# Optimization experiments

Hardware: AMD Instinct MI355X
Metric: run time of the kernel (lower is better)

The kernel has to match this reference:

```python
import jax, jax.numpy as jnp
import numpy as np

H = 12          # num attention heads
DH = 64         # head size (768 / 12)
THRESHOLD = 0.05


def setup_inputs() -> dict:
    key = jax.random.key(0)
    ks = jax.random.split(key, 13)
    B, S, D = 128, 197, 768
    s = 0.02
    return {
        "hidden_states": jax.random.normal(ks[0], (B, S, D), jnp.float32),
        "Wq": jax.random.normal(ks[1], (D, D), jnp.float32) * s,
        "bq": jax.random.normal(ks[2], (D,), jnp.float32) * s,
        "Wk": jax.random.normal(ks[3], (D, D), jnp.float32) * s,
        "bk": jax.random.normal(ks[4], (D,), jnp.float32) * s,
        "Wv": jax.random.normal(ks[5], (D, D), jnp.float32) * s,
        "bv": jax.random.normal(ks[6], (D,), jnp.float32) * s,
        "Wd": jax.random.normal(ks[7], (D, D), jnp.float32) * s,
        "bd": jax.random.normal(ks[8], (D,), jnp.float32) * s,
        "W1": jax.random.normal(ks[9], (D, 64), jnp.float32) * s,
        "b1": jax.random.normal(ks[10], (64,), jnp.float32) * s,
        "W2": jax.random.normal(ks[11], (64, 1), jnp.float32) * s,
        "b2": jax.random.normal(ks[12], (1,), jnp.float32) * s,
    }


def reference(hidden_states, Wq, bq, Wk, bk, Wv, bv, Wd, bd, W1, b1, W2, b2):
    B, S, D = hidden_states.shape
    # --- DHS scoring MLP on patch tokens (exclude CLS), keep_cls=True path ---
    h = jax.nn.relu(hidden_states[:, 1:] @ W1 + b1)        # [B, S-1, 64]
    mlp_out = jax.nn.sigmoid(h @ W2 + b2)[..., 0]          # [B, S-1]
    patch_mask = mlp_out >= THRESHOLD                      # [B, S-1]
    cls_col = jnp.ones((B, 1), dtype=bool)
    mask = jnp.concatenate([cls_col, patch_mask], axis=1)  # [B, S]

    # --- full self-attention; pruning queries only removes rows, keys/values
    # are never pruned, so computing all rows and masking is equivalent ---
    q = (hidden_states @ Wq + bq).reshape(B, S, H, DH)
    k = (hidden_states @ Wk + bk).reshape(B, S, H, DH)
    v = (hidden_states @ Wv + bv).reshape(B, S, H, DH)
    scores = jnp.einsum("bqhd,bkhd->bhqk", q, k) / jnp.sqrt(jnp.float32(DH))
    probs = jax.nn.softmax(scores, axis=-1)                # dropout p=0.0 (eval)
    ctx = jnp.einsum("bhqk,bkhd->bqhd", probs, v).reshape(B, S, D)
    attn_out = (ctx @ Wd + bd) + ctx                       # dense + residual-to-self_outputs

    # scatter-assign: output[i][mask[i]] = attn_out rows for kept tokens
    output = jnp.where(mask[..., None], attn_out, hidden_states)
    return output
```

## Files before the change

### kernel.cpp

```cpp
#include <hip/hip_runtime.h>
#include <hip/hip_bf16.h>

#define HN 12
#define DHD 64
#define BB 128
#define SQ 197
#define DD 768
#define TOK (BB*SQ)
#define SP 224
#define SPS 232

using short8  = __attribute__((ext_vector_type(8))) short;
using floatx4 = __attribute__((ext_vector_type(4))) float;

__device__ __forceinline__ float bf2f(short v) {
    union { unsigned int u; float f; } x;
    x.u = ((unsigned int)(unsigned short)v) << 16;
    return x.f;
}
__device__ __forceinline__ short f2bf(float f) {
    union { float f; unsigned int u; } x; x.f = f;
    unsigned int u = x.u;
    u += 0x7fffu + ((u >> 16) & 1u);
    return (short)(u >> 16);
}
__device__ __forceinline__ float ldf(const void* p, size_t i, bool isf32) {
    return isf32 ? ((const float*)p)[i] : bf2f(((const short*)p)[i]);
}
__device__ __forceinline__ void gload_lds16(const short* g, short* l) {
    __builtin_amdgcn_global_load_lds(
        (const __attribute__((address_space(1))) void*)g,
        (__attribute__((address_space(3))) void*)l, 16, 0, 0);
}

__global__ __launch_bounds__(256) void detect_kernel(
        const short* __restrict__ wq, float* __restrict__ flag) {
    __shared__ int cnt;
    if (threadIdx.x == 0) cnt = 0;
    __syncthreads();
    int local = 0;
    for (int j = 0; j < 16; j++) {
        int i = threadIdx.x * 16 + j;
        unsigned int u = (unsigned short)wq[2 * i];
        unsigned int e = (u >> 7) & 0xFF;
        if (e < 64 || e >= 192) local++;
    }
    for (int d = 1; d < 64; d <<= 1) local += __shfl_xor(local, d, 64);
    if ((threadIdx.x & 63) == 0) atomicAdd(&cnt, local);
    __syncthreads();
    if (threadIdx.x == 0) *flag = (cnt > 256) ? 1.f : 0.f;
}

__global__ void sentinel_kernel(short* out, int n, float code) {
    int i = blockIdx.x * 256 + threadIdx.x;
    if (i < n) out[i] = (i == 0) ? f2bf(code) : (short)0;
}

__global__ __launch_bounds__(256) void prep_kernel(
        const void* __restrict__ Wq, const void* __restrict__ Wk,
        const void* __restrict__ Wv, const void* __restrict__ Wd,
        const void* __restrict__ bq, const void* __restrict__ bk,
        const void* __restrict__ bv, const void* __restrict__ bd,
        const void* __restrict__ W1, const void* __restrict__ b1,
        const void* __restrict__ W2, const void* __restrict__ b2,
        short* __restrict__ WqkvT, short* __restrict__ WdT,
        short* __restrict__ W1T, float* __restrict__ bcat,
        const float* __restrict__ flag) {
    __shared__ short tile[64][72];
    bool isf32 = (*flag != 0.f);
    int blk = blockIdx.x;
    int tid = threadIdx.x;
    int r = tid >> 2, c0 = (tid & 3) << 4;
    const void* W;
    size_t stride;
    int ti, tj, w = 0;
    if (blk < 576) {
        w = blk / 144;
        int t = blk % 144;
        ti = t / 12; tj = t % 12;
        W = (w == 0) ? Wq : (w == 1) ? Wk : (w == 2) ? Wv : Wd;
        stride = DD;
    } else {
        ti = blk - 576; tj = 0;
        W = W1;
        stride = 64;
    }
    for (int c = 0; c < 16; c++)
        tile[r][c0 + c] =
            f2bf(ldf(W, (size_t)(ti * 64 + r) * stride + tj * 64 + c0 + c, isf32));
    __syncthreads();
    short* out;
    if (blk < 576)
        out = (w < 3)
            ? WqkvT + ((size_t)(w * DD + tj * 64 + r)) * DD + ti * 64
            : WdT   + ((size_t)(tj * 64 + r)) * DD + ti * 64;
    else
        out = W1T + (size_t)r * DD + ti * 64;
    for (int h = 0; h < 2; h++) {
        short8 v;
        #pragma unroll
        for (int c = 0; c < 8; c++) v[c] = tile[c0 + h * 8 + c][r];
        *(short8*)&out[c0 + h * 8] = v;
    }
    if (blk == 0) {
        for (int i = tid; i < DD; i += 256) {
            bcat[i]          = ldf(bq, i, isf32);
            bcat[DD + i]     = ldf(bk, i, isf32);
            bcat[2 * DD + i] = ldf(bv, i, isf32);
            bcat[3 * DD + i] = ldf(bd, i, isf32);
        }
        if (tid < 64) {
            bcat[4 * DD + tid]      = ldf(b1, tid, isf32);
            bcat[4 * DD + 64 + tid] = ldf(W2, tid, isf32);
        }
        if (tid == 0) bcat[4 * DD + 128] = ldf(b2, 0, isf32);
    }
}

__global__ __launch_bounds__(256) void mask_gemm(
        const void* __restrict__ hs, const short* __restrict__ W1T,
        const float* __restrict__ bvec, float* __restrict__ mask,
        short* __restrict__ hsb, const float* __restrict__ flag) {
    __shared__ __align__(16) short As[64 * 32];
    __shared__ __align__(16) short Bs[64 * 32];
    bool isf32 = (*flag != 0.f);
    int tid = threadIdx.x, lane = tid & 63, wave = tid >> 6;
    int quad = lane >> 4, l16 = lane & 15;
    int tok0 = blockIdx.x * 64;

    int arow = tid >> 2, achk = tid & 3;
    int acol = ((achk ^ ((arow >> 1) & 3)) << 3);
    const short* Bg = W1T + (size_t)arow * DD +
                      (((achk ^ ((arow >> 1) & 3)) << 3));
    short* Bl = Bs + wave * 512;
    int fcol = ((quad ^ ((l16 >> 1) & 3)) << 3);

    floatx4 acc[4] = {};
    for (int k0 = 0; k0 < DD; k0 += 32) {
        gload_lds16(Bg + k0, Bl);
        size_t gidx = (size_t)(tok0 + arow) * DD + k0 + achk * 8;
        short8 s;
        if (isf32) {
            const float* hf = (const float*)hs;
            float4 f0 = *(const float4*)&hf[gidx];
            float4 f1 = *(const float4*)&hf[gidx + 4];
            s[0]=f2bf(f0.x); s[1]=f2bf(f0.y); s[2]=f2bf(f0.z); s[3]=f2bf(f0.w);
            s[4]=f2bf(f1.x); s[5]=f2bf(f1.y); s[6]=f2bf(f1.z); s[7]=f2bf(f1.w);
        } else {
            s = *(const short8*)&((const short*)hs)[gidx];
        }
        *(short8*)&hsb[gidx] = s;
        *(short8*)&As[(arow << 5) + acol] = s;
        __syncthreads();
        short8 af = *(const short8*)&As[((wave * 16 + l16) << 5) + fcol];
        #pragma unroll
        for (int j = 0; j < 4; j++) {
            short8 bf8 = *(const short8*)&Bs[((j * 16 + l16) << 5) + fcol];
            acc[j] = __builtin_amdgcn_mfma_f32_16x16x32_bf16(af, bf8, acc[j], 0, 0, 0);
        }
        __syncthreads();
    }

    const float* b1f = bvec + 4 * DD;
    const float* w2f = bvec + 4 * DD + 64;
    float b2v = bvec[4 * DD + 128];
    float partial[4] = {0.f, 0.f, 0.f, 0.f};
    #pragma unroll
    for (int j = 0; j < 4; j++) {
        int n = j * 16 + l16;
        float b1v = b1f[n], w2v = w2f[n];
        #pragma unroll
        for (int r = 0; r < 4; r++) {
            float hv = fmaxf(acc[j][r] + b1v, 0.f);
            partial[r] += hv * w2v;
        }
    }
    for (int d = 1; d < 16; d <<= 1)
        #pragma unroll
        for (int r = 0; r < 4; r++)
            partial[r] += __shfl_xor(partial[r], d, 64);
    if (l16 == 0) {
        #pragma unroll
        for (int r = 0; r < 4; r++) {
            int tokr = tok0 + wave * 16 + quad * 4 + r;
            float m = 1.f;
            if (tokr % SQ != 0) {
                float sg = 1.f / (1.f + __expf(-(partial[r] + b2v)));
                m = (sg >= 0.05f) ? 1.f : 0.f;
            }
            mask[tokr] = m;
        }
    }
}

template <int MODE>
__global__ __launch_bounds__(512, 4) void gemm128(
        const short* __restrict__ A, const short* __restrict__ BT,
        const float* __restrict__ bias, void* __restrict__ C,
        int m0g, int Mreal, int N,
        const float* __restrict__ mask, const short* __restrict__ resid,
        const void* __restrict__ hs, const float* __restrict__ flag) {
    constexpr int K = DD;
    constexpr int BK = 64;
    __shared__ __align__(16) short As[128 * BK];
    __shared__ __align__(16) short Bs[128 * BK];
    int tiles_n = N >> 7;
    int nwg = gridDim.x, bid = blockIdx.x;
    int qq = nwg >> 3, rr = nwg & 7, xcd = bid & 7, lid = bid >> 3;
    int wg = (xcd < rr ? xcd * (qq + 1) : rr * (qq + 1) + (xcd - rr) * qq) + lid;
    int bm = wg / tiles_n, bn = wg % tiles_n;
    int m0 = bm << 7, n0 = bn << 7;

    int tid = threadIdx.x, lane = tid & 63, wave = tid >> 6;
    int wx = wave & 3, wy = wave >> 2;
    int quad = lane >> 4, l16 = lane & 15, l7 = l16 & 7;

    int slot0 = (wave << 7) + lane;
    int slot1 = slot0 + 64;
    int r0 = slot0 >> 3, c0s = ((slot0 & 7) ^ (r0 & 7)) << 3;
    int r1 = slot1 >> 3, c1s = ((slot1 & 7) ^ (r1 & 7)) << 3;
    int am0 = m0 + r0; if (am0 >= Mreal) am0 = Mreal - 1;
    int am1 = m0 + r1; if (am1 >= Mreal) am1 = Mreal - 1;
    const short* Ag0 = A + (size_t)am0 * K + c0s;
    const short* Ag1 = A + (size_t)am1 * K + c1s;
    const short* Bg0 = BT + (size_t)(n0 + r0) * K + c0s;
    const short* Bg1 = BT + (size_t)(n0 + r1) * K + c1s;
    short* Al0 = As + wave * 1024;
    short* Al1 = Al0 + 512;
    short* Bl0 = Bs + wave * 1024;
    short* Bl1 = Bl0 + 512;

    floatx4 acc[4][2] = {};
    for (int k0 = 0; k0 < K; k0 += BK) {
        gload_lds16(Ag0 + k0, Al0);
        gload_lds16(Ag1 + k0, Al1);
        gload_lds16(Bg0 + k0, Bl0);
        gload_lds16(Bg1 + k0, Bl1);
        __syncthreads();
        #pragma unroll
        for (int ks = 0; ks < 2; ks++) {
            int colo = ((((ks << 2) + quad) ^ l7) << 3);
            short8 af[4], bfr[2];
            #pragma unroll
            for (int i = 0; i < 4; i++)
                af[i] = *(const short8*)&As[(((wy << 6) + (i << 4) + l16) << 6) + colo];
            #pragma unroll
            for (int j = 0; j < 2; j++)
                bfr[j] = *(const short8*)&Bs[(((wx << 5) + (j << 4) + l16) << 6) + colo];
            #pragma unroll
            for (int i = 0; i < 4; i++)
                #pragma unroll
                for (int j = 0; j < 2; j++)
                    acc[i][j] = __builtin_amdgcn_mfma_f32_16x16x32_bf16(
                        af[i], bfr[j], acc[i][j], 0, 0, 0);
        }
        __syncthreads();
    }

    bool isf32 = (MODE == 1) ? (*flag != 0.f) : false;
    #pragma unroll
    for (int i = 0; i < 4; i++)
        #pragma unroll
        for (int j = 0; j < 2; j++) {
            int n = n0 + (wx << 5) + (j << 4) + l16;
            float bb = bias[n];
            #pragma unroll
            for (int r = 0; r < 4; r++) {
                int m = m0 + (wy << 6) + (i << 4) + (quad << 2) + r;
                if (m >= Mreal) continue;
                float v = acc[i][j][r] + bb;
                if (MODE == 0) {
                    ((short*)C)[(size_t)m * N + n] = f2bf(v);
                } else {
                    size_t gm = (size_t)(m0g + m);
                    v += bf2f(resid[(size_t)m * N + n]);
                    if (mask[gm] == 0.f) v = ldf(hs, gm * N + n, isf32);
                    if (isf32) ((float*)C)[gm * N + n] = v;
                    else       ((short*)C)[gm * N + n] = f2bf(v);
                }
            }
        }
}

__global__ __launch_bounds__(256) void attn_kernel(
        const short* __restrict__ qkv, short* __restrict__ ctx) {
    __shared__ __align__(16) short Vt[DHD * SPS];
    __shared__ __align__(16) short P[4 * 16 * SPS];
    int nwg = gridDim.x, bid = blockIdx.x;
    int qq = nwg >> 3, rr = nwg & 7, xcd = bid & 7, lid = bid >> 3;
    int blk = (xcd < rr ? xcd * (qq + 1) : rr * (qq + 1) + (xcd - rr) * qq) + lid;
    int qc = blk & 3;
    int h  = (blk >> 2) % HN;
    int b  = blk / (4 * HN);
    int tid = threadIdx.x, lane = tid & 63, wave = tid >> 6;
    int quad = lane >> 4, l16 = lane & 15;
    const short* base = qkv + (size_t)b * SQ * 2304;

    for (int i = tid; i < SQ * DHD; i += 256) {
        int s = i >> 6, d = i & 63;
        Vt[d * SPS + s] = base[(size_t)s * 2304 + 1536 + h * 64 + d];
    }
    for (int i = tid; i < (SP - SQ) * DHD; i += 256) {
        int s = SQ + i % (SP - SQ), d = i / (SP - SQ);
        Vt[d * SPS + s] = 0;
    }
    __syncthreads();

    int mrow = qc * 64 + wave * 16 + l16;
    if (mrow > SQ - 1) mrow = SQ - 1;
    const short* Qrow = base + (size_t)mrow * 2304 + h * 64;
    short8 aq0 = *(const short8*)(Qrow + quad * 8);
    short8 aq1 = *(const short8*)(Qrow + 32 + quad * 8);

    floatx4 sc[14];
    for (int t = 0; t < 14; t++) {
        int nrow = t * 16 + l16;
        if (nrow > SQ - 1) nrow = SQ - 1;
        const short* Krow = base + (size_t)nrow * 2304 + DD + h * 64;
        short8 b0 = *(const short8*)(Krow + quad * 8);
        short8 b1 = *(const short8*)(Krow + 32 + quad * 8);
        floatx4 c = {0.f, 0.f, 0.f, 0.f};
        c = __builtin_amdgcn_mfma_f32_16x16x32_bf16(aq0, b0, c, 0, 0, 0);
        c = __builtin_amdgcn_mfma_f32_16x16x32_bf16(aq1, b1, c, 0, 0, 0);
        sc[t] = c;
    }

    const float scale = 0.125f;
    float mx[4] = {-1e30f, -1e30f, -1e30f, -1e30f};
    for (int t = 0; t < 14; t++) {
        int col = t * 16 + l16;
        if (col < SQ)
            for (int r = 0; r < 4; r++) mx[r] = fmaxf(mx[r], sc[t][r]);
    }
    for (int d = 1; d < 16; d <<= 1)
        for (int r = 0; r < 4; r++) mx[r] = fmaxf(mx[r], __shfl_xor(mx[r], d, 64));
    float sum[4] = {0.f, 0.f, 0.f, 0.f};
    for (int t = 0; t < 14; t++) {
        int col = t * 16 + l16;
        for (int r = 0; r < 4; r++) {
            float e = (col < SQ) ? __expf((sc[t][r] - mx[r]) * scale) : 0.f;
            sc[t][r] = e; sum[r] += e;
        }
    }
    for (int d = 1; d < 16; d <<= 1)
        for (int r = 0; r < 4; r++) sum[r] += __shfl_xor(sum[r], d, 64);
    float inv[4];
    for (int r = 0; r < 4; r++) inv[r] = 1.f / sum[r];

    short* Pw = &P[wave * 16 * SPS];
    for (int t = 0; t < 14; t++)
        for (int r = 0; r < 4; r++)
            Pw[(quad * 4 + r) * SPS + t * 16 + l16] = f2bf(sc[t][r] * inv[r]);
    __syncthreads();

    floatx4 co[4] = {};
    for (int ks = 0; ks < 7; ks++) {
        short8 pa = *(const short8*)&Pw[l16 * SPS + ks * 32 + quad * 8];
        for (int j = 0; j < 4; j++) {
            short8 vb = *(const short8*)&Vt[(j * 16 + l16) * SPS + ks * 32 + quad * 8];
            co[j] = __builtin_amdgcn_mfma_f32_16x16x32_bf16(pa, vb, co[j], 0, 0, 0);
        }
    }
    int sq0 = qc * 64 + wave * 16 + quad * 4;
    for (int r = 0; r < 4; r++) {
        int s = sq0 + r;
        if (s < SQ) {
            size_t o = ((size_t)(b * SQ + s)) * DD + h * 64;
            for (int j = 0; j < 4; j++)
                ctx[o + j * 16 + l16] = f2bf(co[j][r]);
        }
    }
}

extern "C" void kernel_launch(void* const* d_in, const int* in_sizes, int n_in,
                              void* d_out, int out_size, void* d_ws, size_t ws_size,
                              hipStream_t stream) {
    const void* hs = d_in[0];
    const void* Wq = d_in[1];
    const void* bq = d_in[2];
    const void* Wk = d_in[3];
    const void* bk = d_in[4];
    const void* Wv = d_in[5];
    const void* bv = d_in[6];
    const void* Wd = d_in[7];
    const void* bd = d_in[8];
    const void* W1 = d_in[9];
    const void* b1 = d_in[10];
    const void* W2 = d_in[11];
    const void* b2 = d_in[12];

    const size_t flag_b  = 16;
    const size_t mask_b  = (size_t)TOK * 4;
    const size_t bcat_b  = (size_t)(4 * DD + 192) * 4;
    const size_t wqkvt_b = (size_t)3 * DD * DD * 2;
    const size_t wdt_b   = (size_t)DD * DD * 2;
    const size_t w1t_b   = (size_t)64 * DD * 2;
    const size_t hsb_b   = (size_t)TOK * DD * 2;
    const size_t fixed   = flag_b + mask_b + bcat_b + wqkvt_b + wdt_b + w1t_b + hsb_b;

    int CHB = 0;
    for (int c = 128; c >= 1; c >>= 1) {
        size_t chtp = (size_t)((c * SQ + 127) / 128) * 128;
        size_t need = fixed + chtp * 2304 * 2 + chtp * DD * 2;
        if (need <= ws_size) { CHB = c; break; }
    }
    if (CHB == 0) {
        sentinel_kernel<<<(out_size + 255) / 256, 256, 0, stream>>>(
            (short*)d_out, out_size, (float)((double)ws_size / 1.0e6));
        return;
    }
    const int CHT  = CHB * SQ;
    const int CHTP = ((CHT + 127) / 128) * 128;

    char* ws = (char*)d_ws;
    float* flag  = (float*)ws;
    float* mask  = (float*)(ws + flag_b);
    float* bcat  = (float*)(ws + flag_b + mask_b);
    short* WqkvT = (short*)(ws + flag_b + mask_b + bcat_b);
    short* WdT   = WqkvT + (size_t)3 * DD * DD;
    short* W1T   = WdT + (size_t)DD * DD;
    short* hsb   = W1T + (size_t)64 * DD;
    short* QKVc  = hsb + (size_t)TOK * DD;
    short* ctxc  = QKVc + (size_t)CHTP * 2304;

    detect_kernel<<<1, 256, 0, stream>>>((const short*)Wq, flag);
    prep_kernel<<<588, 256, 0, stream>>>(Wq, Wk, Wv, Wd, bq, bk, bv, bd,
                                         W1, b1, W2, b2,
                                         WqkvT, WdT, W1T, bcat, flag);
    mask_gemm<<<TOK / 64, 256, 0, stream>>>(hs, W1T, bcat, mask, hsb, flag);

    const int nchunk  = BB / CHB;
    const int tiles_m = CHTP / 128;
    for (int c = 0; c < nchunk; c++) {
        const int m0g = c * CHT;
        gemm128<0><<<tiles_m * (3 * DD / 128), 512, 0, stream>>>(
            hsb + (size_t)m0g * DD, WqkvT, bcat, QKVc,
            m0g, CHT, 3 * DD, nullptr, nullptr, nullptr, flag);
        attn_kernel<<<CHB * HN * 4, 256, 0, stream>>>(QKVc, ctxc);
        gemm128<1><<<tiles_m * (DD / 128), 512, 0, stream>>>(
            ctxc, WdT, bcat + 3 * DD, d_out,
            m0g, CHT, DD, mask, ctxc, hs, flag);
    }
}
```

Measured before the change: 560.4 us.

## Keep attention probabilities in registers via transposed MFMA and lane shuffles

Swaps the MFMA operands so scores come out as K-row by Q-column. Each lane then holds one query's scores, so the softmax max and sum need only two cross-lane shuffles. The normalized probabilities are packed to bf16 with v_cvt_pk_bf16_f32 and redistributed through xor-shuffles straight into the PV MFMA operand layout. This removes the per-wave P tile in LDS and its __syncthreads, and makes the ctx stores packed 8-byte writes. The cost is more shuffle and select instructions plus higher register pressure from the fully unrolled loops.

```diff
diff --git a/kernel.cpp b/kernel.cpp
--- a/kernel.cpp
+++ b/kernel.cpp
@@ -12,6 +12,8 @@
 
 using short8  = __attribute__((ext_vector_type(8))) short;
 using floatx4 = __attribute__((ext_vector_type(4))) float;
+using uintx4  = __attribute__((ext_vector_type(4))) unsigned;
+using uintx2  = __attribute__((ext_vector_type(2))) unsigned;
 
 __device__ __forceinline__ float bf2f(short v) {
     union { unsigned int u; float f; } x;
@@ -31,6 +33,11 @@
     __builtin_amdgcn_global_load_lds(
         (const __attribute__((address_space(1))) void*)g,
         (__attribute__((address_space(3))) void*)l, 16, 0, 0);
+}
+__device__ __forceinline__ unsigned cvtpk(float lo, float hi) {
+    unsigned r;
+    asm volatile("v_cvt_pk_bf16_f32 %0, %1, %2" : "=v"(r) : "v"(lo), "v"(hi));
+    return r;
 }
 
 __global__ __launch_bounds__(256) void detect_kernel(
@@ -285,7 +292,6 @@
 __global__ __launch_bounds__(256) void attn_kernel(
         const short* __restrict__ qkv, short* __restrict__ ctx) {
     __shared__ __align__(16) short Vt[DHD * SPS];
-    __shared__ __align__(16) short P[4 * 16 * SPS];
     int nwg = gridDim.x, bid = blockIdx.x;
     int qq = nwg >> 3, rr = nwg & 7, xcd = bid & 7, lid = bid >> 3;
     int blk = (xcd < rr ? xcd * (qq + 1) : rr * (qq + 1) + (xcd - rr) * qq) + lid;
@@ -309,65 +315,93 @@
     int mrow = qc * 64 + wave * 16 + l16;
     if (mrow > SQ - 1) mrow = SQ - 1;
     const short* Qrow = base + (size_t)mrow * 2304 + h * 64;
-    short8 aq0 = *(const short8*)(Qrow + quad * 8);
-    short8 aq1 = *(const short8*)(Qrow + 32 + quad * 8);
-
-    floatx4 sc[14];
-    for (int t = 0; t < 14; t++) {
+    short8 bq0 = *(const short8*)(Qrow + quad * 8);
+    short8 bq1 = *(const short8*)(Qrow + 32 + quad * 8);
+
+    floatx4 sc[13];
+    #pragma unroll
+    for (int t = 0; t < 13; t++) {
         int nrow = t * 16 + l16;
         if (nrow > SQ - 1) nrow = SQ - 1;
         const short* Krow = base + (size_t)nrow * 2304 + DD + h * 64;
-        short8 b0 = *(const short8*)(Krow + quad * 8);
-        short8 b1 = *(const short8*)(Krow + 32 + quad * 8);
+        short8 ka0 = *(const short8*)(Krow + quad * 8);
+        short8 ka1 = *(const short8*)(Krow + 32 + quad * 8);
         floatx4 c = {0.f, 0.f, 0.f, 0.f};
-        c = __builtin_amdgcn_mfma_f32_16x16x32_bf16(aq0, b0, c, 0, 0, 0);
-        c = __builtin_amdgcn_mfma_f32_16x16x32_bf16(aq1, b1, c, 0, 0, 0);
+        c = __builtin_amdgcn_mfma_f32_16x16x32_bf16(ka0, bq0, c, 0, 0, 0);
+        c = __builtin_amdgcn_mfma_f32_16x16x32_bf16(ka1, bq1, c, 0, 0, 0);
         sc[t] = c;
     }
 
     const float scale = 0.125f;
-    float mx[4] = {-1e30f, -1e30f, -1e30f, -1e30f};
-    for (int t = 0; t < 14; t++) {
-        int col = t * 16 + l16;
-        if (col < SQ)
-            for (int r = 0; r < 4; r++) mx[r] = fmaxf(mx[r], sc[t][r]);
-    }
-    for (int d = 1; d < 16; d <<= 1)
-        for (int r = 0; r < 4; r++) mx[r] = fmaxf(mx[r], __shfl_xor(mx[r], d, 64));
-    float sum[4] = {0.f, 0.f, 0.f, 0.f};
-    for (int t = 0; t < 14; t++) {
-        int col = t * 16 + l16;
+    float mx = -1e30f;
+    #pragma unroll
+    for (int t = 0; t < 12; t++)
+        #pragma unroll
+        for (int r = 0; r < 4; r++) mx = fmaxf(mx, sc[t][r]);
+    #pragma unroll
+    for (int r = 0; r < 4; r++)
+        mx = fmaxf(mx, (4 * quad + r < 5) ? sc[12][r] : -1e30f);
+    mx = fmaxf(mx, __shfl_xor(mx, 16, 64));
+    mx = fmaxf(mx, __shfl_xor(mx, 32, 64));
+    float sum = 0.f;
+    #pragma unroll
+    for (int t = 0; t < 12; t++)
+        #pragma unroll
         for (int r = 0; r < 4; r++) {
-            float e = (col < SQ) ? __expf((sc[t][r] - mx[r]) * scale) : 0.f;
-            sc[t][r] = e; sum[r] += e;
-        }
-    }
-    for (int d = 1; d < 16; d <<= 1)
-        for (int r = 0; r < 4; r++) sum[r] += __shfl_xor(sum[r], d, 64);
-    float inv[4];
-    for (int r = 0; r < 4; r++) inv[r] = 1.f / sum[r];
-
-    short* Pw = &P[wave * 16 * SPS];
-    for (int t = 0; t < 14; t++)
-        for (int r = 0; r < 4; r++)
-            Pw[(quad * 4 + r) * SPS + t * 16 + l16] = f2bf(sc[t][r] * inv[r]);
-    __syncthreads();
-
+            float e = __expf((sc[t][r] - mx) * scale);
+            sc[t][r] = e; sum += e;
+        }
+    #pragma unroll
+    for (int r = 0; r < 4; r++) {
+        float e = (4 * quad + r < 5) ? __expf((sc[12][r] - mx) * scale) : 0.f;
+        sc[12][r] = e; sum += e;
+    }
+    sum += __shfl_xor(sum, 16, 64);
+    sum += __shfl_xor(sum, 32, 64);
+    float inv = 1.f / sum;
+
+    unsigned pklo[14], pkhi[14];
+    #pragma unroll
+    for (int t = 0; t < 13; t++) {
+        pklo[t] = cvtpk(sc[t][0] * inv, sc[t][1] * inv);
+        pkhi[t] = cvtpk(sc[t][2] * inv, sc[t][3] * inv);
+    }
+    pklo[13] = 0u; pkhi[13] = 0u;
+
+    int c0 = quad & 1, par = quad >> 1;
     floatx4 co[4] = {};
-    for (int ks = 0; ks < 7; ks++) {
-        short8 pa = *(const short8*)&Pw[l16 * SPS + ks * 32 + quad * 8];
+    #pragma unroll
+    for (int u = 0; u < 7; u++) {
+        int t0 = 2 * u, t1 = 2 * u + 1;
+        unsigned eol = par ? pklo[t1] : pklo[t0];
+        unsigned eoh = par ? pkhi[t1] : pkhi[t0];
+        unsigned exl = par ? pklo[t0] : pklo[t1];
+        unsigned exh = par ? pkhi[t0] : pkhi[t1];
+        unsigned a16l = __shfl_xor(eol, 16, 64), a16h = __shfl_xor(eoh, 16, 64);
+        unsigned a32l = __shfl_xor(exl, 32, 64), a32h = __shfl_xor(exh, 32, 64);
+        unsigned a48l = __shfl_xor(exl, 48, 64), a48h = __shfl_xor(exh, 48, 64);
+        uintx4 fw;
+        fw[0] = c0 ? (par ? a16l : a48l) : (par ? a32l : eol);
+        fw[1] = c0 ? (par ? a16h : a48h) : (par ? a32h : eoh);
+        fw[2] = c0 ? (par ? eol : a32l) : (par ? a48l : a16l);
+        fw[3] = c0 ? (par ? eoh : a32h) : (par ? a48h : a16h);
+        short8 pa = __builtin_bit_cast(short8, fw);
+        #pragma unroll
         for (int j = 0; j < 4; j++) {
-            short8 vb = *(const short8*)&Vt[(j * 16 + l16) * SPS + ks * 32 + quad * 8];
-            co[j] = __builtin_amdgcn_mfma_f32_16x16x32_bf16(pa, vb, co[j], 0, 0, 0);
-        }
-    }
-    int sq0 = qc * 64 + wave * 16 + quad * 4;
-    for (int r = 0; r < 4; r++) {
-        int s = sq0 + r;
-        if (s < SQ) {
-            size_t o = ((size_t)(b * SQ + s)) * DD + h * 64;
-            for (int j = 0; j < 4; j++)
-                ctx[o + j * 16 + l16] = f2bf(co[j][r]);
+            short8 vb = *(const short8*)&Vt[(j * 16 + l16) * SPS + u * 32 + quad * 8];
+            co[j] = __builtin_amdgcn_mfma_f32_16x16x32_bf16(vb, pa, co[j], 0, 0, 0);
+        }
+    }
+
+    int sq = qc * 64 + wave * 16 + l16;
+    if (sq < SQ) {
+        size_t o = ((size_t)(b * SQ + sq)) * DD + h * 64;
+        #pragma unroll
+        for (int j = 0; j < 4; j++) {
+            uintx2 w;
+            w[0] = cvtpk(co[j][0], co[j][1]);
+            w[1] = cvtpk(co[j][2], co[j][3]);
+            *reinterpret_cast<uintx2*>(&ctx[o + j * 16 + quad * 4]) = w;
         }
     }
 }
```

Result: faster. 531.0 us (-5.2%).
